# Kernel tuning notes

Measured on AMD Instinct MI355X. Metric: run time of the kernel, lower is better.

Reference implementation:

```python
import jax, jax.numpy as jnp
import numpy as np

D = 512
H = 8
DH = D // H
FF = 2 * D
EPS = 1e-5


def _layernorm(x, g, b):
    mu = jnp.mean(x, axis=-1, keepdims=True)
    var = jnp.mean(jnp.square(x - mu), axis=-1, keepdims=True)
    return (x - mu) * jax.lax.rsqrt(var + EPS) * g + b


def setup_inputs() -> dict:
    key = jax.random.key(0)
    ks = jax.random.split(key, 8)
    s = 0.02
    x = jax.random.normal(ks[0], (1, 4096, D), dtype=jnp.float32)
    w_qkv = jax.random.normal(ks[1], (D, 3 * D), dtype=jnp.float32) * s
    b_qkv = jnp.zeros((3 * D,), jnp.float32)
    w_out = jax.random.normal(ks[2], (D, D), dtype=jnp.float32) * s
    b_out = jnp.zeros((D,), jnp.float32)
    w_ff1 = jax.random.normal(ks[3], (D, FF), dtype=jnp.float32) * s
    b_ff1 = jnp.zeros((FF,), jnp.float32)
    w_ff2 = jax.random.normal(ks[4], (FF, D), dtype=jnp.float32) * s
    b_ff2 = jnp.zeros((D,), jnp.float32)
    g1 = jnp.ones((D,), jnp.float32)
    bt1 = jnp.zeros((D,), jnp.float32)
    g2 = jnp.ones((D,), jnp.float32)
    bt2 = jnp.zeros((D,), jnp.float32)
    return {"x": x, "w_qkv": w_qkv, "b_qkv": b_qkv, "w_out": w_out, "b_out": b_out,
            "w_ff1": w_ff1, "b_ff1": b_ff1, "w_ff2": w_ff2, "b_ff2": b_ff2,
            "g1": g1, "bt1": bt1, "g2": g2, "bt2": bt2}


def reference(x, w_qkv, b_qkv, w_out, b_out, w_ff1, b_ff1, w_ff2, b_ff2, g1, bt1, g2, bt2):
    B, S, _ = x.shape
    h = _layernorm(x, g1, bt1)
    qkv = h @ w_qkv + b_qkv                      # [B,S,3D]
    qkv = qkv.reshape(B, S, 3, H, DH)
    q, k, v = qkv[:, :, 0], qkv[:, :, 1], qkv[:, :, 2]   # [B,S,H,DH]
    scores = jnp.einsum('bqhd,bkhd->bhqk', q, k) / np.sqrt(DH).astype(np.float32)
    causal = jnp.tril(jnp.ones((S, S), dtype=bool))
    scores = jnp.where(causal, scores, -jnp.inf)
    attn = jax.nn.softmax(scores, axis=-1)
    out = jnp.einsum('bhqk,bkhd->bqhd', attn, v).reshape(B, S, D)
    x = x + out @ w_out + b_out
    h2 = _layernorm(x, g2, bt2)
    ff = jax.nn.gelu(h2 @ w_ff1 + b_ff1, approximate=False) @ w_ff2 + b_ff2
    return x + ff
```

## Files before the change

kernel.cpp:

```cpp
#include <hip/hip_runtime.h>
#include <math.h>

#define D 512
#define H 8
#define DH 64
#define S 4096
#define FF 1024

typedef __attribute__((ext_vector_type(8))) short bf16x8;
typedef __attribute__((ext_vector_type(4))) float f32x4;
typedef __attribute__((ext_vector_type(16))) float f32x16;

__device__ __forceinline__ unsigned short f2bf(float f) {
    union { float f; unsigned u; } c; c.f = f;
    unsigned r = (c.u + 0x7fff + ((c.u >> 16) & 1)) >> 16;
    return (unsigned short)r;
}
__device__ __forceinline__ float bf2f(unsigned short u) {
    union { unsigned u; float f; } c; c.u = ((unsigned)u) << 16;
    return c.f;
}
__device__ __forceinline__ unsigned asu(float f) {
    union { float f; unsigned u; } c; c.f = f; return c.u;
}

__device__ __forceinline__ void gl_lds16(const void* g, void* l) {
    __builtin_amdgcn_global_load_lds(
        (const __attribute__((address_space(1))) void*)g,
        (__attribute__((address_space(3))) void*)l, 16, 0, 0);
}

__global__ __launch_bounds__(256) void transpose_all(const float* __restrict__ wqkv,
                                                     const float* __restrict__ wout,
                                                     const float* __restrict__ wff1,
                                                     const float* __restrict__ wff2,
                                                     unsigned short* __restrict__ oqkv,
                                                     unsigned short* __restrict__ oout,
                                                     unsigned short* __restrict__ off1,
                                                     unsigned short* __restrict__ off2) {
    __shared__ unsigned short tile[32][33];
    int id = blockIdx.x;
    const float* src; unsigned short* dst; int K, N, lid;
    if (id < 768)       { src = wqkv; dst = oqkv; K = 512;  N = 1536; lid = id; }
    else if (id < 1024) { src = wout; dst = oout; K = 512;  N = 512;  lid = id - 768; }
    else if (id < 1536) { src = wff1; dst = off1; K = 512;  N = 1024; lid = id - 1024; }
    else                { src = wff2; dst = off2; K = 1024; N = 512;  lid = id - 1536; }
    int nb = N / 32;
    int n0 = (lid % nb) * 32, k0 = (lid / nb) * 32;
    int tx = threadIdx.x & 31, ty = threadIdx.x >> 5;
#pragma unroll
    for (int i = 0; i < 32; i += 8)
        tile[ty + i][tx] = f2bf(src[(size_t)(k0 + ty + i) * N + n0 + tx]);
    __syncthreads();
#pragma unroll
    for (int i = 0; i < 32; i += 8)
        dst[(size_t)(n0 + ty + i) * K + k0 + tx] = tile[tx][ty + i];
}

__global__ __launch_bounds__(256) void transpose_v(const unsigned short* __restrict__ qkv,
                                                   unsigned short* __restrict__ vT) {
    __shared__ unsigned short tile[32][33];
    int s0 = blockIdx.x * 32, d0 = blockIdx.y * 32;
    int tx = threadIdx.x & 31, ty = threadIdx.x >> 5;
#pragma unroll
    for (int i = 0; i < 32; i += 8)
        tile[ty + i][tx] = qkv[(size_t)(s0 + ty + i) * (3 * D) + 2 * D + d0 + tx];
    __syncthreads();
#pragma unroll
    for (int i = 0; i < 32; i += 8)
        vT[(size_t)(d0 + ty + i) * S + s0 + tx] = tile[tx][ty + i];
}

__global__ __launch_bounds__(256) void ln_kernel(const float* __restrict__ x,
                                                 const float* __restrict__ g,
                                                 const float* __restrict__ bta,
                                                 unsigned short* __restrict__ out) {
    int row = blockIdx.x, tid = threadIdx.x;
    const float* xr = x + (size_t)row * D;
    float2 v = *(const float2*)(xr + tid * 2);
    float s = v.x + v.y;
    float sq = v.x * v.x + v.y * v.y;
#pragma unroll
    for (int m = 1; m < 64; m <<= 1) { s += __shfl_xor(s, m); sq += __shfl_xor(sq, m); }
    __shared__ float red[8];
    int wave = tid >> 6, lane = tid & 63;
    if (lane == 0) { red[wave] = s; red[4 + wave] = sq; }
    __syncthreads();
    s = red[0] + red[1] + red[2] + red[3];
    sq = red[4] + red[5] + red[6] + red[7];
    float mu = s * (1.f / D);
    float var = sq * (1.f / D) - mu * mu;
    float rstd = rsqrtf(var + 1e-5f);
    int i = tid * 2;
    float2 gg = *(const float2*)(g + i);
    float2 bb = *(const float2*)(bta + i);
    out[(size_t)row * D + i]     = f2bf((v.x - mu) * rstd * gg.x + bb.x);
    out[(size_t)row * D + i + 1] = f2bf((v.y - mu) * rstd * gg.y + bb.y);
}

enum { EPI_BF16 = 0, EPI_RESID_F32 = 1, EPI_GELU_BF16 = 2 };

template <int EPI, int WMI>
__global__ __launch_bounds__(256, WMI == 4 ? 3 : 4)
void gemm2_kernel(const unsigned short* __restrict__ A,
                  const unsigned short* __restrict__ BT,
                  const float* __restrict__ bias,
                  const float* __restrict__ resid,
                  void* __restrict__ out,
                  int M, int N, int K) {
    constexpr int BM = 32 * WMI;
    constexpr int BN = 128;
    constexpr int APH = BM * 8 / 256;
    __shared__ __align__(16) unsigned short sA[BM * 64];
    __shared__ __align__(16) unsigned short sB[BN * 64];

    int tid = threadIdx.x;
    int wave = tid >> 6, lane = tid & 63;
    int quad = lane >> 4, l16 = lane & 15;
    int lx = l16 & 7;
    int wr = (wave >> 1) * (BM / 2), wc = (wave & 1) * 64;
    int m0 = blockIdx.y * BM, n0 = blockIdx.x * BN;

    f32x4 acc[WMI][4];
#pragma unroll
    for (int i = 0; i < WMI; i++)
#pragma unroll
        for (int j = 0; j < 4; j++) acc[i][j] = (f32x4){0.f, 0.f, 0.f, 0.f};

    int srow = tid >> 3;
    int spc = tid & 7;
    int scc = spc ^ (srow & 7);
    const unsigned short* Abase = A + (size_t)(m0 + srow) * K + scc * 8;
    const unsigned short* Bbase = BT + (size_t)(n0 + srow) * K + scc * 8;
    unsigned short* sAdst = sA + (tid & ~63) * 8;
    unsigned short* sBdst = sB + (tid & ~63) * 8;

    for (int k0 = 0; k0 < K; k0 += 64) {
        __syncthreads();
#pragma unroll
        for (int ph = 0; ph < APH; ph++)
            gl_lds16(Abase + (size_t)(ph * 32) * K + k0, sAdst + ph * 256 * 8);
#pragma unroll
        for (int ph = 0; ph < 4; ph++)
            gl_lds16(Bbase + (size_t)(ph * 32) * K + k0, sBdst + ph * 256 * 8);
        asm volatile("s_waitcnt vmcnt(0)" ::: "memory");
        __syncthreads();

#pragma unroll
        for (int ks = 0; ks < 2; ks++) {
            int cxs = ((ks * 4 + quad) ^ lx) * 8;
            bf16x8 af[WMI], bfr[4];
#pragma unroll
            for (int mi = 0; mi < WMI; mi++)
                af[mi] = *(const bf16x8*)(sA + (wr + mi * 16 + l16) * 64 + cxs);
#pragma unroll
            for (int ni = 0; ni < 4; ni++)
                bfr[ni] = *(const bf16x8*)(sB + (wc + ni * 16 + l16) * 64 + cxs);
#pragma unroll
            for (int mi = 0; mi < WMI; mi++)
#pragma unroll
                for (int ni = 0; ni < 4; ni++)
                    acc[mi][ni] = __builtin_amdgcn_mfma_f32_16x16x32_bf16(af[mi], bfr[ni], acc[mi][ni], 0, 0, 0);
        }
    }

#pragma unroll
    for (int mi = 0; mi < WMI; mi++)
#pragma unroll
        for (int ni = 0; ni < 4; ni++) {
            int col = n0 + wc + ni * 16 + l16;
            float bs = bias[col];
#pragma unroll
            for (int r = 0; r < 4; r++) {
                int row = m0 + wr + mi * 16 + quad * 4 + r;
                float v = acc[mi][ni][r] + bs;
                size_t idx = (size_t)row * N + col;
                if constexpr (EPI == EPI_RESID_F32) {
                    ((float*)out)[idx] = v + resid[idx];
                } else if constexpr (EPI == EPI_GELU_BF16) {
                    v = 0.5f * v * (1.f + erff(v * 0.70710678118f));
                    ((unsigned short*)out)[idx] = f2bf(v);
                } else {
                    ((unsigned short*)out)[idx] = f2bf(v);
                }
            }
        }
}

#define LDF 72
#define LDO 68

__global__ __launch_bounds__(256, 4) void flash6_kernel(const unsigned short* __restrict__ qkv,
                                                        const unsigned short* __restrict__ vT,
                                                        unsigned short* __restrict__ O_part,
                                                        float* __restrict__ l_part) {
    __shared__ __align__(16) unsigned short sK[2][64 * LDF];
    __shared__ __align__(16) unsigned short sV[2][64 * LDF];

    int tid = threadIdx.x;
    int w = tid >> 6, lane = tid & 63;
    int lq = lane & 31, hb = lane >> 5;

    int h = blockIdx.x & 7;
    int u = blockIdx.x >> 3;
    int Q = 31, c = 0, acc = 0;
    for (int qq = 31; qq >= 0; --qq) {
        int n = (qq >> 2) + 1;
        if (u < acc + n) { Q = qq; c = u - acc; break; }
        acc += n;
    }
    int T = 2 * Q + 2;
    int t0c = c * 8;
    int t1c = min(t0c + 8, T);
    int q0w = Q * 128 + w * 32;
    int qrow = q0w + lq;
    int qmax = q0w + 31;

    const float CEXP = 0.18033688f;

    bf16x8 qf[4];
#pragma unroll
    for (int dc = 0; dc < 4; dc++) {
        bf16x8 qraw = *(const bf16x8*)(qkv + (size_t)qrow * (3 * D) + h * DH + dc * 16 + hb * 8);
        bf16x8 qs;
#pragma unroll
        for (int j = 0; j < 8; j++)
            qs[j] = (short)f2bf(bf2f((unsigned short)qraw[j]) * CEXP);
        qf[dc] = qs;
    }

    f32x16 oa[2];
#pragma unroll
    for (int i = 0; i < 16; i++) { oa[0][i] = 0.f; oa[1][i] = 0.f; }
    float l4[4] = {0.f, 0.f, 0.f, 0.f};

    int rr = tid >> 3;
    int cc8 = (tid & 7) * 8;
    const unsigned short* kgb = qkv + (size_t)rr * (3 * D) + D + h * DH + cc8;
    const unsigned short* vgb = vT + (size_t)(h * DH + rr) * S + cc8;

    bf16x8 gk0, gk1, gv0, gv1;
    auto glb = [&](int t) {
        const unsigned short* kg = kgb + (size_t)t * 64 * (3 * D);
        gk0 = *(const bf16x8*)(kg);
        gk1 = *(const bf16x8*)(kg + (size_t)32 * (3 * D));
        const unsigned short* vg = vgb + t * 64;
        gv0 = *(const bf16x8*)(vg);
        gv1 = *(const bf16x8*)(vg + (size_t)32 * S);
    };

    glb(t0c);
    for (int t = t0c; t < t1c; ++t) {
        int buf = (t - t0c) & 1;
        unsigned short* dk = &sK[buf][rr * LDF + cc8];
        *(bf16x8*)dk = gk0;
        *(bf16x8*)(dk + 32 * LDF) = gk1;
        unsigned short* dv = &sV[buf][rr * LDF + cc8];
        *(bf16x8*)dv = gv0;
        *(bf16x8*)(dv + 32 * LDF) = gv1;
        if (t + 1 < t1c) glb(t + 1);
        __syncthreads();

        if (64 * t > qmax) continue;

        f32x16 sa[2];
#pragma unroll
        for (int i = 0; i < 16; i++) { sa[0][i] = 0.f; sa[1][i] = 0.f; }
#pragma unroll
        for (int kt = 0; kt < 2; kt++)
#pragma unroll
            for (int dc = 0; dc < 4; dc++) {
                bf16x8 kf = *(const bf16x8*)(&sK[buf][(kt * 32 + lq) * LDF + dc * 16 + hb * 8]);
                sa[kt] = __builtin_amdgcn_mfma_f32_32x32x16_bf16(kf, qf[dc], sa[kt], 0, 0, 0);
            }

        bool dmask = (64 * t + 63 > qmax);
        unsigned p2[2][8];
        if (!dmask) {
#pragma unroll
            for (int kt = 0; kt < 2; kt++) {
                float e[16];
#pragma unroll
                for (int r = 0; r < 16; r++) {
                    e[r] = __builtin_amdgcn_exp2f(sa[kt][r]);
                    l4[r & 3] += e[r];
                }
#pragma unroll
                for (int p = 0; p < 8; p++)
                    p2[kt][p] = __builtin_amdgcn_perm(asu(e[2 * p + 1]) + 0x8000u,
                                                      asu(e[2 * p]) + 0x8000u, 0x07060302u);
            }
        } else {
#pragma unroll
            for (int kt = 0; kt < 2; kt++) {
                float e[16];
#pragma unroll
                for (int r = 0; r < 16; r++) {
                    float v = __builtin_amdgcn_exp2f(sa[kt][r]);
                    int key = 64 * t + kt * 32 + (r & 3) + 8 * (r >> 2) + 4 * hb;
                    if (key > qrow) v = 0.f;
                    e[r] = v;
                    l4[r & 3] += v;
                }
#pragma unroll
                for (int p = 0; p < 8; p++)
                    p2[kt][p] = __builtin_amdgcn_perm(asu(e[2 * p + 1]) + 0x8000u,
                                                      asu(e[2 * p]) + 0x8000u, 0x07060302u);
            }
        }

#pragma unroll
        for (int kc = 0; kc < 4; kc++) {
            int kt = kc >> 1;
            int b0i = (kc & 1) * 4;
            unsigned a0 = p2[kt][b0i + 0], a1 = p2[kt][b0i + 1];
            unsigned b0 = p2[kt][b0i + 2], b1 = p2[kt][b0i + 3];
            unsigned s0 = hb ? a0 : b0, s1 = hb ? a1 : b1;
            unsigned x0 = __shfl_xor(s0, 32), x1 = __shfl_xor(s1, 32);
            unsigned l0 = hb ? b0 : a0, l1 = hb ? b1 : a1;
            union { unsigned u[4]; bf16x8 v; } fr;
            fr.u[0] = hb ? x0 : l0;
            fr.u[1] = hb ? x1 : l1;
            fr.u[2] = hb ? l0 : x0;
            fr.u[3] = hb ? l1 : x1;
#pragma unroll
            for (int dt = 0; dt < 2; dt++) {
                bf16x8 vf = *(const bf16x8*)(&sV[buf][(dt * 32 + lq) * LDF + kc * 16 + hb * 8]);
                oa[dt] = __builtin_amdgcn_mfma_f32_32x32x16_bf16(vf, fr.v, oa[dt], 0, 0, 0);
            }
        }
    }

    float lsum = (l4[0] + l4[1]) + (l4[2] + l4[3]);
    lsum += __shfl_xor(lsum, 32);
    if (hb == 0)
        l_part[((size_t)c * H + h) * S + q0w + lq] = lsum;

    __syncthreads();
    unsigned short* sOw = (unsigned short*)sK + w * 32 * LDO;
#pragma unroll
    for (int kt = 0; kt < 2; kt++)
#pragma unroll
        for (int r = 0; r < 16; r++) {
            int d = kt * 32 + (r & 3) + 8 * (r >> 2) + 4 * hb;
            sOw[lq * LDO + d] = f2bf(oa[kt][r]);
        }
    asm volatile("s_waitcnt lgkmcnt(0)" ::: "memory");
    unsigned short* Op = O_part + ((size_t)c * S + q0w) * D + h * DH;
#pragma unroll
    for (int it = 0; it < 4; it++) {
        int rq = (lane >> 3) + it * 8;
        bf16x8 val = *(const bf16x8*)(sOw + rq * LDO + (lane & 7) * 8);
        *(bf16x8*)(Op + (size_t)rq * D + (lane & 7) * 8) = val;
    }
}

__global__ __launch_bounds__(256) void norm_kernel(const unsigned short* __restrict__ O_part,
                                                   const float* __restrict__ l_part,
                                                   unsigned short* __restrict__ O) {
    int idx = blockIdx.x * 256 + threadIdx.x;
    int row = idx >> 9, col = idx & 511;
    int h = col >> 6;
    int nch = ((row >> 7) >> 2) + 1;
    float o = 0.f, l = 0.f;
    for (int cc = 0; cc < nch; cc++) {
        o += bf2f(O_part[((size_t)cc * S + row) * D + col]);
        l += l_part[((size_t)cc * H + h) * S + row];
    }
    O[idx] = f2bf(o / l);
}

extern "C" void kernel_launch(void* const* d_in, const int* in_sizes, int n_in,
                              void* d_out, int out_size, void* d_ws, size_t ws_size,
                              hipStream_t stream) {
    const float* x     = (const float*)d_in[0];
    const float* w_qkv = (const float*)d_in[1];
    const float* b_qkv = (const float*)d_in[2];
    const float* w_out = (const float*)d_in[3];
    const float* b_out = (const float*)d_in[4];
    const float* w_ff1 = (const float*)d_in[5];
    const float* b_ff1 = (const float*)d_in[6];
    const float* w_ff2 = (const float*)d_in[7];
    const float* b_ff2 = (const float*)d_in[8];
    const float* g1    = (const float*)d_in[9];
    const float* bt1   = (const float*)d_in[10];
    const float* g2    = (const float*)d_in[11];
    const float* bt2   = (const float*)d_in[12];

    char* ws = (char*)d_ws;
    size_t off = 0;
    auto alloc = [&](size_t bytes) {
        void* p = ws + off;
        off += (bytes + 255) & ~(size_t)255;
        return p;
    };
    unsigned short* hbuf   = (unsigned short*)alloc((size_t)S * D * 2);
    unsigned short* qkvbuf = (unsigned short*)alloc((size_t)S * 3 * D * 2);
    unsigned short* vTbuf  = (unsigned short*)alloc((size_t)D * S * 2);
    unsigned short* Obuf   = (unsigned short*)alloc((size_t)S * D * 2);
    unsigned short* wqkvT  = (unsigned short*)alloc((size_t)3 * D * D * 2);
    unsigned short* woutT  = (unsigned short*)alloc((size_t)D * D * 2);
    unsigned short* wff1T  = (unsigned short*)alloc((size_t)FF * D * 2);
    unsigned short* wff2T  = (unsigned short*)alloc((size_t)D * FF * 2);
    unsigned short* Opart  = (unsigned short*)alloc((size_t)8 * S * D * 2);
    float*          lpart  = (float*)alloc((size_t)8 * H * S * 4);
    unsigned short* h2buf  = hbuf;
    unsigned short* ff1buf = qkvbuf;
    float*          x2buf  = (float*)Opart;

    transpose_all<<<dim3(2048), 256, 0, stream>>>(w_qkv, w_out, w_ff1, w_ff2,
                                                  wqkvT, woutT, wff1T, wff2T);

    ln_kernel<<<S, 256, 0, stream>>>(x, g1, bt1, hbuf);
    gemm2_kernel<EPI_BF16, 2><<<dim3(12, 64), 256, 0, stream>>>(
        hbuf, wqkvT, b_qkv, nullptr, qkvbuf, S, 3 * D, D);
    transpose_v<<<dim3(S / 32, D / 32), 256, 0, stream>>>(qkvbuf, vTbuf);
    flash6_kernel<<<dim3(1152), 256, 0, stream>>>(qkvbuf, vTbuf, Opart, lpart);
    norm_kernel<<<dim3(S * D / 256), 256, 0, stream>>>(Opart, lpart, Obuf);
    gemm2_kernel<EPI_RESID_F32, 2><<<dim3(4, 64), 256, 0, stream>>>(
        Obuf, woutT, b_out, x, x2buf, S, D, D);
    ln_kernel<<<S, 256, 0, stream>>>(x2buf, g2, bt2, h2buf);
    gemm2_kernel<EPI_GELU_BF16, 2><<<dim3(8, 64), 256, 0, stream>>>(
        h2buf, wff1T, b_ff1, nullptr, ff1buf, S, FF, D);
    gemm2_kernel<EPI_RESID_F32, 2><<<dim3(4, 64), 256, 0, stream>>>(
        ff1buf, wff2T, b_ff2, x2buf, (float*)d_out, S, D, FF);
}
```

Measured before the change: 205.2 us.

## Deepen flash K/V prefetch to two tiles ahead and enlarge QKV/FF1 GEMM tiles

```diff
diff --git a/kernel.cpp b/kernel.cpp
--- a/kernel.cpp
+++ b/kernel.cpp
@@ -190,7 +190,7 @@
 #define LDF 72
 #define LDO 68
 
-__global__ __launch_bounds__(256, 4) void flash6_kernel(const unsigned short* __restrict__ qkv,
+__global__ __launch_bounds__(256, 4) void flash7_kernel(const unsigned short* __restrict__ qkv,
                                                         const unsigned short* __restrict__ vT,
                                                         unsigned short* __restrict__ O_part,
                                                         float* __restrict__ l_part) {
@@ -239,29 +239,30 @@
     const unsigned short* kgb = qkv + (size_t)rr * (3 * D) + D + h * DH + cc8;
     const unsigned short* vgb = vT + (size_t)(h * DH + rr) * S + cc8;
 
-    bf16x8 gk0, gk1, gv0, gv1;
-    auto glb = [&](int t) {
+    bf16x8 kA[2], vA[2], kB[2], vB[2], kC[2], vC[2];
+
+    auto glb = [&](bf16x8 (&kf)[2], bf16x8 (&vf)[2], int t) {
         const unsigned short* kg = kgb + (size_t)t * 64 * (3 * D);
-        gk0 = *(const bf16x8*)(kg);
-        gk1 = *(const bf16x8*)(kg + (size_t)32 * (3 * D));
+        kf[0] = *(const bf16x8*)(kg);
+        kf[1] = *(const bf16x8*)(kg + (size_t)32 * (3 * D));
         const unsigned short* vg = vgb + t * 64;
-        gv0 = *(const bf16x8*)(vg);
-        gv1 = *(const bf16x8*)(vg + (size_t)32 * S);
+        vf[0] = *(const bf16x8*)(vg);
+        vf[1] = *(const bf16x8*)(vg + (size_t)32 * S);
     };
 
-    glb(t0c);
-    for (int t = t0c; t < t1c; ++t) {
+    auto step = [&](bf16x8 (&kf)[2], bf16x8 (&vf)[2],
+                    bf16x8 (&pk)[2], bf16x8 (&pv)[2], int t) {
         int buf = (t - t0c) & 1;
         unsigned short* dk = &sK[buf][rr * LDF + cc8];
-        *(bf16x8*)dk = gk0;
-        *(bf16x8*)(dk + 32 * LDF) = gk1;
+        *(bf16x8*)dk = kf[0];
+        *(bf16x8*)(dk + 32 * LDF) = kf[1];
         unsigned short* dv = &sV[buf][rr * LDF + cc8];
-        *(bf16x8*)dv = gv0;
-        *(bf16x8*)(dv + 32 * LDF) = gv1;
-        if (t + 1 < t1c) glb(t + 1);
+        *(bf16x8*)dv = vf[0];
+        *(bf16x8*)(dv + 32 * LDF) = vf[1];
+        if (t + 2 < t1c) glb(pk, pv, t + 2);
         __syncthreads();
 
-        if (64 * t > qmax) continue;
+        if (64 * t > qmax) return;
 
         f32x16 sa[2];
 #pragma unroll
@@ -270,8 +271,8 @@
         for (int kt = 0; kt < 2; kt++)
 #pragma unroll
             for (int dc = 0; dc < 4; dc++) {
-                bf16x8 kf = *(const bf16x8*)(&sK[buf][(kt * 32 + lq) * LDF + dc * 16 + hb * 8]);
-                sa[kt] = __builtin_amdgcn_mfma_f32_32x32x16_bf16(kf, qf[dc], sa[kt], 0, 0, 0);
+                bf16x8 kfr = *(const bf16x8*)(&sK[buf][(kt * 32 + lq) * LDF + dc * 16 + hb * 8]);
+                sa[kt] = __builtin_amdgcn_mfma_f32_32x32x16_bf16(kfr, qf[dc], sa[kt], 0, 0, 0);
             }
 
         bool dmask = (64 * t + 63 > qmax);
@@ -325,10 +326,19 @@
             fr.u[3] = hb ? l1 : x1;
 #pragma unroll
             for (int dt = 0; dt < 2; dt++) {
-                bf16x8 vf = *(const bf16x8*)(&sV[buf][(dt * 32 + lq) * LDF + kc * 16 + hb * 8]);
-                oa[dt] = __builtin_amdgcn_mfma_f32_32x32x16_bf16(vf, fr.v, oa[dt], 0, 0, 0);
+                bf16x8 vfr = *(const bf16x8*)(&sV[buf][(dt * 32 + lq) * LDF + kc * 16 + hb * 8]);
+                oa[dt] = __builtin_amdgcn_mfma_f32_32x32x16_bf16(vfr, fr.v, oa[dt], 0, 0, 0);
             }
         }
+    };
+
+    glb(kA, vA, t0c);
+    if (t0c + 1 < t1c) glb(kB, vB, t0c + 1);
+    int t = t0c;
+    while (true) {
+        step(kA, vA, kC, vC, t); if (++t == t1c) break;
+        step(kB, vB, kA, vA, t); if (++t == t1c) break;
+        step(kC, vC, kB, vB, t); if (++t == t1c) break;
     }
 
     float lsum = (l4[0] + l4[1]) + (l4[2] + l4[3]);
@@ -412,15 +422,15 @@
                                                   wqkvT, woutT, wff1T, wff2T);
 
     ln_kernel<<<S, 256, 0, stream>>>(x, g1, bt1, hbuf);
-    gemm2_kernel<EPI_BF16, 2><<<dim3(12, 64), 256, 0, stream>>>(
+    gemm2_kernel<EPI_BF16, 4><<<dim3(12, 32), 256, 0, stream>>>(
         hbuf, wqkvT, b_qkv, nullptr, qkvbuf, S, 3 * D, D);
     transpose_v<<<dim3(S / 32, D / 32), 256, 0, stream>>>(qkvbuf, vTbuf);
-    flash6_kernel<<<dim3(1152), 256, 0, stream>>>(qkvbuf, vTbuf, Opart, lpart);
+    flash7_kernel<<<dim3(1152), 256, 0, stream>>>(qkvbuf, vTbuf, Opart, lpart);
     norm_kernel<<<dim3(S * D / 256), 256, 0, stream>>>(Opart, lpart, Obuf);
     gemm2_kernel<EPI_RESID_F32, 2><<<dim3(4, 64), 256, 0, stream>>>(
         Obuf, woutT, b_out, x, x2buf, S, D, D);
     ln_kernel<<<S, 256, 0, stream>>>(x2buf, g2, bt2, h2buf);
-    gemm2_kernel<EPI_GELU_BF16, 2><<<dim3(8, 64), 256, 0, stream>>>(
+    gemm2_kernel<EPI_GELU_BF16, 4><<<dim3(8, 32), 256, 0, stream>>>(
         h2buf, wff1T, b_ff1, nullptr, ff1buf, S, FF, D);
     gemm2_kernel<EPI_RESID_F32, 2><<<dim3(4, 64), 256, 0, stream>>>(
         ff1buf, wff2T, b_ff2, x2buf, (float*)d_out, S, D, FF);
```

New measurement: 251.4 us. 1.23x slower.
